# Kernel optimization log

Measured on AMD Instinct MI355X. Metric: run time of the kernel, lower is better.

## Reference

```python
import jax, jax.numpy as jnp
import numpy as np

B, C, H, W, K = 64, 64, 32, 32, 512  # batch, embedding_dim, latent HxW, num_embeddings
COMMITMENT_COST = 0.25


def setup_inputs() -> dict:
    key = jax.random.key(0)
    k1, k2 = jax.random.split(key)
    inputs = jax.random.normal(k1, (B, C, H, W), dtype=jnp.float32)
    # nn.Embedding weight initialized uniform(-1/K, 1/K)
    weight = jax.random.uniform(k2, (K, C), minval=-1.0 / K, maxval=1.0 / K, dtype=jnp.float32)
    return {"inputs": inputs, "weight": weight}


def reference(inputs, weight):
    # NCHW -> NHWC
    x = jnp.transpose(inputs, (0, 2, 3, 1))  # [B,H,W,C]
    b, h, w, c = x.shape
    flat = x.reshape(-1, c)  # [N, C], N = B*H*W

    distances = (jnp.sum(flat * flat, axis=1, keepdims=True)
                 + jnp.sum(weight * weight, axis=1)[None, :]
                 - 2.0 * flat @ weight.T)

    idx = jnp.argmin(distances, axis=1)  # [N]
    encodings = jax.nn.one_hot(idx, weight.shape[0], dtype=flat.dtype)  # [N, K]

    # gather codebook vectors (same math as encodings @ weight)
    quantized = weight[idx].reshape(x.shape)  # [B,H,W,C]

    e_latent = jnp.mean((jax.lax.stop_gradient(quantized) - x) ** 2, axis=(1, 2, 3))
    q_latent = jnp.mean((quantized - jax.lax.stop_gradient(x)) ** 2, axis=(1, 2, 3))
    loss = q_latent + COMMITMENT_COST * e_latent  # [B]

    # straight-through estimator
    quantized_st = x + jax.lax.stop_gradient(quantized - x)

    avg_probs = jnp.mean(encodings, axis=0)  # [K]
    perplexity = jnp.exp(-jnp.sum(avg_probs * jnp.log(avg_probs + 1e-10)))

    q_out = jnp.transpose(quantized_st, (0, 3, 1, 2))  # back to NCHW
    enc_idx = idx.reshape(b, -1)  # [B, H*W]
    return (q_out, loss, perplexity, encodings, enc_idx, distances)
```

## Files before the change

kernel.cpp:

```cpp
#include <hip/hip_runtime.h>
#include <stdint.h>
#include <math.h>

#pragma clang fp contract(off)

#define B_   64
#define C_   64
#define HW_  1024
#define K_   512
#define N_   65536

#define OUT_Q    0ull
#define OUT_LOSS 4194304ull
#define OUT_PERP 4194368ull
#define OUT_ENC  4194369ull
#define OUT_IDX  37748801ull
#define OUT_DIST 37814337ull

#define WS_WT     0ull
#define WS_WT2    131072ull
#define WS_WNORM  262144ull
#define WS_SUMSQ  264192ull

__global__ __launch_bounds__(256) void vq_prep(const float* __restrict__ w,
                                               float* __restrict__ wt,
                                               float* __restrict__ wt2,
                                               float* __restrict__ wnorm,
                                               float* __restrict__ sumsq) {
  const int t = threadIdx.x;
  const int g = blockIdx.x * 256 + t;
  const int c = g >> 9;
  const int k = g & 511;
  const float v = w[k * 64 + c];
  wt[g] = v;
  wt2[(c >> 4) * 8192 + (c & 15) * 512 + (k & 63) * 8 + (k >> 6)] = v;

  if (blockIdx.x == 0 && t < 64) sumsq[t] = 0.f;

  if (blockIdx.x < 16) {
    const int row = g >> 3;
    const int j = g & 7;
    float s = 0.f;
    for (int i = 0; i < 8; ++i) {
      float vv = w[row * 64 + 8 * i + j];
      float sq = vv * vv;
      s = s + sq;
    }
    float o1 = __shfl_xor(s, 1); s = s + o1;
    float o2 = __shfl_xor(s, 2); s = s + o2;
    float o4 = __shfl_xor(s, 4); s = s + o4;
    if (j == 0) wnorm[row] = s;
  }
}

__global__ __launch_bounds__(256, 3) void vq_main(const float* __restrict__ x,
                                                  const float* __restrict__ wt,
                                                  const float* __restrict__ wt2,
                                                  const float* __restrict__ wnorm,
                                                  float* __restrict__ out,
                                                  float* __restrict__ sumsq) {
  __shared__ float x_s[64 * 32];
  __shared__ float w_s[16 * 512];
  __shared__ float wn_s[512];
  __shared__ float an_s[32];
  __shared__ int   kmin_s[32];
  __shared__ float red_s[4];

  const int t   = threadIdx.x;
  const int blk = blockIdx.x;
  const int n0  = blk * 32;
  const int b   = n0 >> 10;
  const int hw0 = n0 & 1023;
  const int wid = t >> 6;
  const int l   = t & 63;

  {
    const float* xb = x + (size_t)b * 65536 + hw0;
    const int c0 = t >> 3;
    const int m4 = (t & 7) * 4;
    for (int i = 0; i < 2; ++i) {
      int c = i * 32 + c0;
      float4 v = *(const float4*)(xb + (size_t)c * 1024 + m4);
      *(float4*)(&x_s[c * 32 + m4]) = v;
    }
  }
  wn_s[t] = wnorm[t];
  wn_s[t + 256] = wnorm[t + 256];
  __syncthreads();

  {
    const int r = t >> 3, j = t & 7;
    float s = 0.f;
    for (int i = 0; i < 8; ++i) {
      float v = x_s[(8 * i + j) * 32 + r];
      float sq = v * v;
      s = s + sq;
    }
    float o1 = __shfl_xor(s, 1); s = s + o1;
    float o2 = __shfl_xor(s, 2); s = s + o2;
    float o4 = __shfl_xor(s, 4); s = s + o4;
    if (j == 0) an_s[r] = s;
  }

  float wn[8];
  for (int j = 0; j < 8; ++j) wn[j] = wn_s[l + 64 * j];

  const int uwid = __builtin_amdgcn_readfirstlane(wid);
  const float* xrow = x + (size_t)b * 65536 + (size_t)(hw0 + 8 * uwid);

  float acc[8][8];
  for (int i = 0; i < 8; ++i)
    for (int j = 0; j < 8; ++j) acc[i][j] = 0.f;

#pragma unroll 1
  for (int cc = 0; cc < 4; ++cc) {
    __syncthreads();
    for (int i = 0; i < 8; ++i) {
      int f4 = i * 256 + t;
      *(float4*)(&w_s[f4 * 4]) = *(const float4*)(wt2 + (size_t)cc * 8192 + f4 * 4);
    }
    __syncthreads();
#pragma unroll
    for (int cl = 0; cl < 16; ++cl) {
      const float* xp = xrow + (size_t)(cc * 16 + cl) * 1024;
      float xv[8];
      *(float4*)(xv)     = *(const float4*)(xp);
      *(float4*)(xv + 4) = *(const float4*)(xp + 4);
      float wv[8];
      *(float4*)(wv)     = *(const float4*)(&w_s[cl * 512 + l * 8]);
      *(float4*)(wv + 4) = *(const float4*)(&w_s[cl * 512 + l * 8 + 4]);
      for (int i = 0; i < 8; ++i)
        for (int j = 0; j < 8; ++j)
          acc[i][j] = __builtin_fmaf(xv[i], wv[j], acc[i][j]);
    }
  }

  float* const dist_o = out + OUT_DIST;
  float* const enc_o  = out + OUT_ENC;
  const int m_base = 8 * wid;
  for (int i = 0; i < 8; ++i) {
    const int m = m_base + i;
    const size_t n = (size_t)(n0 + m);
    const float an = an_s[m];
    float D[8];
    for (int j = 0; j < 8; ++j) {
      float tt = an + wn[j];
      D[j] = __builtin_fmaf(-2.f, acc[i][j], tt);
    }
    float vb = D[0]; int kb = l;
    for (int j = 1; j < 8; ++j) {
      if (D[j] < vb) { vb = D[j]; kb = l + 64 * j; }
    }
    for (int d = 1; d < 64; d <<= 1) {
      float v2 = __shfl_xor(vb, d);
      int   k2 = __shfl_xor(kb, d);
      if (v2 < vb || (v2 == vb && k2 < kb)) { vb = v2; kb = k2; }
    }
    const size_t rb = n * 512 + l;
    for (int j = 0; j < 8; ++j) dist_o[rb + 64 * j] = D[j];
    for (int j = 0; j < 8; ++j) enc_o[rb + 64 * j] = (l + 64 * j == kb) ? 1.f : 0.f;
    if (l == i) {
      out[OUT_IDX + n] = (float)kb;
      kmin_s[m] = kb;
    }
  }
  __syncthreads();

  float lsum = 0.f;
  float* const q_o = out + OUT_Q;
  for (int it = 0; it < 8; ++it) {
    const int idx8 = it * 256 + t;
    const int c = idx8 >> 5, m = idx8 & 31;
    const int kb = kmin_s[m];
    const float qv = wt[(size_t)c * 512 + kb];
    const float xv = x_s[c * 32 + m];
    const float d = qv - xv;
    lsum = __builtin_fmaf(d, d, lsum);
    q_o[(size_t)b * 65536 + (size_t)c * 1024 + (hw0 + m)] = qv;
  }
  for (int d = 1; d < 64; d <<= 1) lsum += __shfl_xor(lsum, d);
  if (l == 0) red_s[wid] = lsum;
  __syncthreads();
  if (t == 0) {
    float s = (red_s[0] + red_s[1]) + (red_s[2] + red_s[3]);
    atomicAdd(sumsq + b, s);
  }
}

__global__ __launch_bounds__(1024) void vq_fin(float* __restrict__ out,
                                               const float* __restrict__ sumsq) {
  __shared__ int h4[4 * 512];
  __shared__ double red[8];
  const int t = threadIdx.x;
  h4[t] = 0; h4[t + 1024] = 0;
  __syncthreads();
  const float* idxp = out + OUT_IDX;
  int* const myh = &h4[(t & 3) * 512];
  for (int i = t; i < 65536; i += 1024) {
    int k = (int)idxp[i];
    atomicAdd(&myh[k], 1);
  }
  __syncthreads();
  if (t < 512) {
    int cnt = h4[t] + h4[512 + t] + h4[1024 + t] + h4[1536 + t];
    double p = (double)cnt * (1.0 / 65536.0);
    double term = p * log(p + 1e-10);
    for (int d = 1; d < 64; d <<= 1) term += __shfl_xor(term, d);
    if ((t & 63) == 0) red[t >> 6] = term;
  }
  __syncthreads();
  if (t == 0) {
    double s = 0.0;
    for (int i = 0; i < 8; ++i) s += red[i];
    out[OUT_PERP] = (float)exp(-s);
  }
  if (t < 64) {
    float m = sumsq[t] * (1.0f / 65536.0f);
    out[OUT_LOSS + t] = m + 0.25f * m;
  }
}

extern "C" void kernel_launch(void* const* d_in, const int* in_sizes, int n_in,
                              void* d_out, int out_size, void* d_ws, size_t ws_size,
                              hipStream_t stream) {
  const float* x = (const float*)d_in[0];
  const float* w = (const float*)d_in[1];
  float* out = (float*)d_out;
  char* ws = (char*)d_ws;
  float* wt    = (float*)(ws + WS_WT);
  float* wt2   = (float*)(ws + WS_WT2);
  float* wnorm = (float*)(ws + WS_WNORM);
  float* sumsq = (float*)(ws + WS_SUMSQ);

  vq_prep<<<128, 256, 0, stream>>>(w, wt, wt2, wnorm, sumsq);
  vq_main<<<2048, 256, 0, stream>>>(x, wt, wt2, wnorm, out, sumsq);
  vq_fin<<<1, 1024, 0, stream>>>(out, sumsq);
}
```

Before: 365.3 us.

## Read x from LDS in GEMM, nontemporal stores, stage quantized via LDS transpose

The inner product loop now reads x from the already-staged shared tile instead of reloading it from global memory. The large distance and one-hot outputs use nontemporal stores to avoid polluting the cache. The quantized codebook rows are gathered coalesced from the original weight into a padded shared buffer, which reuses the weight tile space, and written out as float4. This drops the transposed wt copy from the workspace. It adds an extra barrier and LDS traffic in the epilogue.

```diff
diff --git a/kernel.cpp b/kernel.cpp
--- a/kernel.cpp
+++ b/kernel.cpp
@@ -3,12 +3,6 @@
 #include <math.h>
 
 #pragma clang fp contract(off)
-
-#define B_   64
-#define C_   64
-#define HW_  1024
-#define K_   512
-#define N_   65536
 
 #define OUT_Q    0ull
 #define OUT_LOSS 4194304ull
@@ -17,13 +11,11 @@
 #define OUT_IDX  37748801ull
 #define OUT_DIST 37814337ull
 
-#define WS_WT     0ull
-#define WS_WT2    131072ull
-#define WS_WNORM  262144ull
-#define WS_SUMSQ  264192ull
+#define WS_WT2    0ull
+#define WS_WNORM  131072ull
+#define WS_SUMSQ  133120ull
 
 __global__ __launch_bounds__(256) void vq_prep(const float* __restrict__ w,
-                                               float* __restrict__ wt,
                                                float* __restrict__ wt2,
                                                float* __restrict__ wnorm,
                                                float* __restrict__ sumsq) {
@@ -31,9 +23,7 @@
   const int g = blockIdx.x * 256 + t;
   const int c = g >> 9;
   const int k = g & 511;
-  const float v = w[k * 64 + c];
-  wt[g] = v;
-  wt2[(c >> 4) * 8192 + (c & 15) * 512 + (k & 63) * 8 + (k >> 6)] = v;
+  wt2[(c >> 4) * 8192 + (c & 15) * 512 + (k & 63) * 8 + (k >> 6)] = w[k * 64 + c];
 
   if (blockIdx.x == 0 && t < 64) sumsq[t] = 0.f;
 
@@ -54,16 +44,15 @@
 }
 
 __global__ __launch_bounds__(256, 3) void vq_main(const float* __restrict__ x,
-                                                  const float* __restrict__ wt,
+                                                  const float* __restrict__ w,
                                                   const float* __restrict__ wt2,
                                                   const float* __restrict__ wnorm,
                                                   float* __restrict__ out,
                                                   float* __restrict__ sumsq) {
   __shared__ float x_s[64 * 32];
-  __shared__ float w_s[16 * 512];
+  __shared__ float pool[16 * 512];
   __shared__ float wn_s[512];
   __shared__ float an_s[32];
-  __shared__ int   kmin_s[32];
   __shared__ float red_s[4];
 
   const int t   = threadIdx.x;
@@ -105,9 +94,6 @@
   float wn[8];
   for (int j = 0; j < 8; ++j) wn[j] = wn_s[l + 64 * j];
 
-  const int uwid = __builtin_amdgcn_readfirstlane(wid);
-  const float* xrow = x + (size_t)b * 65536 + (size_t)(hw0 + 8 * uwid);
-
   float acc[8][8];
   for (int i = 0; i < 8; ++i)
     for (int j = 0; j < 8; ++j) acc[i][j] = 0.f;
@@ -117,23 +103,25 @@
     __syncthreads();
     for (int i = 0; i < 8; ++i) {
       int f4 = i * 256 + t;
-      *(float4*)(&w_s[f4 * 4]) = *(const float4*)(wt2 + (size_t)cc * 8192 + f4 * 4);
+      *(float4*)(&pool[f4 * 4]) = *(const float4*)(wt2 + (size_t)cc * 8192 + f4 * 4);
     }
     __syncthreads();
 #pragma unroll
     for (int cl = 0; cl < 16; ++cl) {
-      const float* xp = xrow + (size_t)(cc * 16 + cl) * 1024;
+      const float* xp = &x_s[(cc * 16 + cl) * 32 + 8 * wid];
       float xv[8];
       *(float4*)(xv)     = *(const float4*)(xp);
       *(float4*)(xv + 4) = *(const float4*)(xp + 4);
       float wv[8];
-      *(float4*)(wv)     = *(const float4*)(&w_s[cl * 512 + l * 8]);
-      *(float4*)(wv + 4) = *(const float4*)(&w_s[cl * 512 + l * 8 + 4]);
+      *(float4*)(wv)     = *(const float4*)(&pool[cl * 512 + l * 8]);
+      *(float4*)(wv + 4) = *(const float4*)(&pool[cl * 512 + l * 8 + 4]);
       for (int i = 0; i < 8; ++i)
         for (int j = 0; j < 8; ++j)
           acc[i][j] = __builtin_fmaf(xv[i], wv[j], acc[i][j]);
     }
   }
+  __syncthreads();
+  float* const q_s = pool;
 
   float* const dist_o = out + OUT_DIST;
   float* const enc_o  = out + OUT_ENC;
@@ -157,26 +145,34 @@
       if (v2 < vb || (v2 == vb && k2 < kb)) { vb = v2; kb = k2; }
     }
     const size_t rb = n * 512 + l;
-    for (int j = 0; j < 8; ++j) dist_o[rb + 64 * j] = D[j];
-    for (int j = 0; j < 8; ++j) enc_o[rb + 64 * j] = (l + 64 * j == kb) ? 1.f : 0.f;
-    if (l == i) {
-      out[OUT_IDX + n] = (float)kb;
-      kmin_s[m] = kb;
-    }
+    for (int j = 0; j < 8; ++j)
+      __builtin_nontemporal_store(D[j], &dist_o[rb + 64 * j]);
+    for (int j = 0; j < 8; ++j)
+      __builtin_nontemporal_store((l + 64 * j == kb) ? 1.f : 0.f,
+                                  &enc_o[rb + 64 * j]);
+    if (l == i) out[OUT_IDX + n] = (float)kb;
+    q_s[m * 65 + l] = w[(size_t)kb * 64 + l];
   }
   __syncthreads();
 
   float lsum = 0.f;
   float* const q_o = out + OUT_Q;
-  for (int it = 0; it < 8; ++it) {
-    const int idx8 = it * 256 + t;
-    const int c = idx8 >> 5, m = idx8 & 31;
-    const int kb = kmin_s[m];
-    const float qv = wt[(size_t)c * 512 + kb];
-    const float xv = x_s[c * 32 + m];
-    const float d = qv - xv;
-    lsum = __builtin_fmaf(d, d, lsum);
-    q_o[(size_t)b * 65536 + (size_t)c * 1024 + (hw0 + m)] = qv;
+  {
+    const int c0 = t >> 3;
+    const int m4 = (t & 7) * 4;
+    for (int h = 0; h < 2; ++h) {
+      const int c = h * 32 + c0;
+      float qv[4];
+      for (int e = 0; e < 4; ++e) qv[e] = q_s[(m4 + e) * 65 + c];
+      float4 xv4 = *(const float4*)(&x_s[c * 32 + m4]);
+      const float xe[4] = {xv4.x, xv4.y, xv4.z, xv4.w};
+      for (int e = 0; e < 4; ++e) {
+        float d = qv[e] - xe[e];
+        lsum = __builtin_fmaf(d, d, lsum);
+      }
+      float4 qv4 = {qv[0], qv[1], qv[2], qv[3]};
+      *(float4*)(&q_o[(size_t)b * 65536 + (size_t)c * 1024 + (hw0 + m4)]) = qv4;
+    }
   }
   for (int d = 1; d < 64; d <<= 1) lsum += __shfl_xor(lsum, d);
   if (l == 0) red_s[wid] = lsum;
@@ -227,12 +223,11 @@
   const float* w = (const float*)d_in[1];
   float* out = (float*)d_out;
   char* ws = (char*)d_ws;
-  float* wt    = (float*)(ws + WS_WT);
   float* wt2   = (float*)(ws + WS_WT2);
   float* wnorm = (float*)(ws + WS_WNORM);
   float* sumsq = (float*)(ws + WS_SUMSQ);
 
-  vq_prep<<<128, 256, 0, stream>>>(w, wt, wt2, wnorm, sumsq);
-  vq_main<<<2048, 256, 0, stream>>>(x, wt, wt2, wnorm, out, sumsq);
+  vq_prep<<<128, 256, 0, stream>>>(w, wt2, wnorm, sumsq);
+  vq_main<<<2048, 256, 0, stream>>>(x, w, wt2, wnorm, out, sumsq);
   vq_fin<<<1, 1024, 0, stream>>>(out, sumsq);
 }
```

After: 358.7 us. No clear change (-1.8%).
